# Optimization experiments

Hardware: AMD Instinct MI355X
Metric: run time of the kernel (lower is better)

Reference implementation:

```python
import jax, jax.numpy as jnp
import numpy as np
from jax import lax

DILATIONS = (1, 3, 9, 27, 81, 1)
C = 128        # model channels
UP = 2048      # up-projection channels
K = 512        # filterbank kernel size
NZ = 64        # non_zero_elements kept by sparsify
B = 2
N = 32768      # n_samples


def conv1d(x, w, b, dilation=1, padding='VALID'):
    # x: [B,Cin,T], w: [Cout,Cin,Kw]
    y = lax.conv_general_dilated(x, w, (1,), padding, rhs_dilation=(dilation,),
                                 dimension_numbers=('NCH', 'OIH', 'NCH'))
    return y if b is None else y + b[None, :, None]


def dilated_stack(x, ws, bs, causal_past):
    # residual stack of kernel-2 dilated causal convs; 'only-past' pads left, 'only-future' pads right
    for i, d in enumerate(DILATIONS):
        pad = ((0, 0), (0, 0), (d, 0)) if causal_past else ((0, 0), (0, 0), (0, d))
        h = conv1d(jnp.pad(x, pad), ws[i], bs[i], dilation=d)
        x = x + jax.nn.leaky_relu(h, 0.2)
    return x


def sparsify_topk(x, k):
    # keep top-k values (soft=True: keep magnitudes) over flattened (C,T) per sample
    b = x.shape[0]
    flat = x.reshape(b, -1)
    vals, idx = lax.top_k(flat, k)
    out = jnp.zeros_like(flat).at[jnp.arange(b)[:, None], idx].set(vals)
    return out.reshape(x.shape)


def setup_inputs() -> dict:
    key = jax.random.key(0)
    ks = jax.random.split(key, 11)
    s = 0.1  # weight_init
    return {
        'x': jax.random.normal(ks[0], (B, 1, N), jnp.float32),
        'fb': jax.random.normal(ks[1], (C, 1, K), jnp.float32) * s,        # filterbank
        'enc_w': jax.random.normal(ks[2], (6, C, C, 2), jnp.float32) * s,
        'enc_b': jnp.zeros((6, C), jnp.float32),
        'up_w': jax.random.normal(ks[3], (UP, C, 1), jnp.float32) * s,
        'up_b': jnp.zeros((UP,), jnp.float32),
        'down_w': jax.random.normal(ks[4], (C, UP, 1), jnp.float32) * s,
        'down_b': jnp.zeros((C,), jnp.float32),
        'dec_w': jax.random.normal(ks[5], (6, C, C, 2), jnp.float32) * s,
        'dec_b': jnp.zeros((6, C), jnp.float32),
    }


def reference(x, fb, enc_w, enc_b, up_w, up_b, down_w, down_b, dec_w, dec_b):
    # filterbank analysis: [B,1,N] -> [B,C,N]
    spec = conv1d(x, fb, None, 1, ((K // 2, K // 2 - 1),))
    enc = dilated_stack(spec, enc_w, enc_b, causal_past=False)  # 'only-future'
    enc = conv1d(enc, up_w, up_b)            # [B,2048,N]
    enc = sparsify_topk(enc, NZ)             # 64 nonzeros per sample
    enc = conv1d(enc, down_w, down_b)        # [B,128,N]
    dec = dilated_stack(enc, dec_w, dec_b, causal_past=True)    # 'only-past'
    dec = jnp.pad(dec, ((0, 0), (0, 0), (0, 1)))                # F.pad(decoded, (0,1))
    # transposed convolve back to waveform: flipped filterbank, sum over channels
    kt = jnp.flip(fb, -1).transpose(1, 0, 2)  # [1,C,K]
    final = conv1d(dec, kt, None, 1, ((K // 2 - 1, K // 2),))[:, :, :N]
    return final
```

## Files before the change

kernel.cpp:

```cpp
#include <hip/hip_runtime.h>
#include <stdint.h>

#define NB  2
#define NC  128
#define NT  32768
#define KFB 512
#define NUP 2048
#define CAP 14336

typedef unsigned int u32;
typedef unsigned short u16;
typedef short s16;
typedef float f32x4 __attribute__((ext_vector_type(4)));
typedef s16 short8 __attribute__((ext_vector_type(8)));
typedef u32 u32x4 __attribute__((ext_vector_type(4)));
typedef u32 u32x2 __attribute__((ext_vector_type(2)));

__device__ __forceinline__ u32 f2key(float v){
  u32 u = __float_as_uint(v);
  return (u & 0x80000000u) ? ~u : (u | 0x80000000u);
}
__device__ __forceinline__ float key2f(u32 k){
  u32 u = (k & 0x80000000u) ? (k & 0x7FFFFFFFu) : ~k;
  return __uint_as_float(u);
}
__device__ __forceinline__ u16 bf16rn(float v){
  u32 u = __float_as_uint(v);
  return (u16)((u + 0x7FFFu + ((u>>16)&1u)) >> 16);
}
__device__ __forceinline__ u32 packhl(float v){
  u16 h = bf16rn(v);
  u16 lo = bf16rn(v - __uint_as_float(((u32)h)<<16));
  return ((u32)h<<16) | lo;
}

#define RSH 136

__global__ __launch_bounds__(256) void k_prep(const float* __restrict__ encw,
    const float* __restrict__ decw, const float* __restrict__ upw,
    const float* __restrict__ fbw,
    u16* __restrict__ wdil, u16* __restrict__ wup, u16* __restrict__ wfb,
    u32* __restrict__ h1, u32* __restrict__ h2, int* __restrict__ counts){
  int g = blockIdx.x*256 + threadIdx.x;
  if (g < 2048) h1[g] = 0u;
  else if (g < 4096) h2[g-2048] = 0u;
  if (g < NB) counts[g] = 0;
  if (g < 49152){
    int l = g & 63, mt = (g>>6)&7, s = (g>>9)&7, layer = g>>12;
    const float* W = (layer < 6) ? (encw + (size_t)layer*NC*NC*2)
                                 : (decw + (size_t)(layer-6)*NC*NC*2);
    int co = mt*16 + (l & 15);
    int kb = s*32 + ((l>>4)<<3);
    union { u16 h[8]; u32x4 q; } H, L;
    #pragma unroll
    for (int j=0;j<8;++j){
      int k = kb + j;
      float v = W[((size_t)co*NC + (k&127))*2 + (k>>7)];
      u16 h = bf16rn(v);
      H.h[j] = h;
      L.h[j] = bf16rn(v - __uint_as_float(((u32)h)<<16));
    }
    int unit = g >> 6;
    *(u32x4*)(wdil + (size_t)unit*1024 + (l<<3)) = H.q;
    *(u32x4*)(wdil + (size_t)unit*1024 + 512 + (l<<3)) = L.q;
  } else if (g < 81920){
    int g2 = g - 49152;
    int l = g2 & 63, umt = (g2>>6)&127, s = g2>>13;
    int u = umt*16 + (l & 15);
    int kb = s*32 + ((l>>4)<<3);
    union { u16 h[8]; u32x4 q; } H, L;
    #pragma unroll
    for (int j=0;j<8;++j){
      float v = upw[(size_t)u*NC + kb + j];
      u16 h = bf16rn(v);
      H.h[j] = h;
      L.h[j] = bf16rn(v - __uint_as_float(((u32)h)<<16));
    }
    int unit = g2 >> 6;
    *(u32x4*)(wup + (size_t)unit*1024 + (l<<3)) = H.q;
    *(u32x4*)(wup + (size_t)unit*1024 + 512 + (l<<3)) = L.q;
  } else if (g < 90112){
    int g3 = g - 81920;
    int l = g3 & 63, mt = (g3>>6)&7, s = g3>>9;
    int c = mt*16 + (l & 15);
    int kb = s*32 + ((l>>4)<<3);
    union { u16 h[8]; u32x4 q; } H, L;
    #pragma unroll
    for (int j=0;j<8;++j){
      float v = fbw[(size_t)c*KFB + kb + j];
      u16 h = bf16rn(v);
      H.h[j] = h;
      L.h[j] = bf16rn(v - __uint_as_float(((u32)h)<<16));
    }
    int unit = g3 >> 6;
    *(u32x4*)(wfb + (size_t)unit*1024 + (l<<3)) = H.q;
    *(u32x4*)(wfb + (size_t)unit*1024 + 512 + (l<<3)) = L.q;
  }
}

__global__ __launch_bounds__(256) void k_fb(const float* __restrict__ x,
    const u16* __restrict__ wfb, float* __restrict__ spec){
  __shared__ u32 xw[640];
  const int tid = threadIdx.x;
  const int t0 = blockIdx.x << 7;
  const int b  = blockIdx.y;
  const int lane = tid & 63, w = tid >> 6;
  const int wy = w >> 1, wx = w & 1;
  const int quad = lane >> 4, l15 = lane & 15;
  for (int i = tid; i < 640; i += 256){
    int t = t0 - 256 + i;
    float v = ((u32)t < (u32)NT) ? x[b*NT + t] : 0.0f;
    xw[i] = packhl(v);
  }
  __syncthreads();
  f32x4 acc[4][4] = {};
  for (int s = 0; s < 16; ++s){
    short8 ah[4], al[4];
    #pragma unroll
    for (int mt=0; mt<4; ++mt){
      const u16* p = wfb + (size_t)(s*8 + wy*4 + mt)*1024 + (lane<<3);
      ah[mt] = *(const short8*)p;
      al[mt] = *(const short8*)(p + 512);
    }
    short8 xh[4], xl[4];
    #pragma unroll
    for (int nt=0; nt<4; ++nt){
      int base = s*32 + quad*8 + (wx<<6) + (nt<<4) + l15;
      u32 r[8];
      #pragma unroll
      for (int j=0;j<8;++j) r[j] = xw[base + j];
      union { u32 u[4]; short8 v; } H, L;
      H.u[0] = __builtin_amdgcn_perm(r[1], r[0], 0x07060302u);
      H.u[1] = __builtin_amdgcn_perm(r[3], r[2], 0x07060302u);
      H.u[2] = __builtin_amdgcn_perm(r[5], r[4], 0x07060302u);
      H.u[3] = __builtin_amdgcn_perm(r[7], r[6], 0x07060302u);
      L.u[0] = __builtin_amdgcn_perm(r[1], r[0], 0x05040100u);
      L.u[1] = __builtin_amdgcn_perm(r[3], r[2], 0x05040100u);
      L.u[2] = __builtin_amdgcn_perm(r[5], r[4], 0x05040100u);
      L.u[3] = __builtin_amdgcn_perm(r[7], r[6], 0x05040100u);
      xh[nt] = H.v; xl[nt] = L.v;
    }
    #pragma unroll
    for (int mt=0; mt<4; ++mt){
      #pragma unroll
      for (int nt=0; nt<4; ++nt){
        acc[mt][nt] = __builtin_amdgcn_mfma_f32_16x16x32_bf16(ah[mt], xh[nt], acc[mt][nt], 0,0,0);
        acc[mt][nt] = __builtin_amdgcn_mfma_f32_16x16x32_bf16(ah[mt], xl[nt], acc[mt][nt], 0,0,0);
        acc[mt][nt] = __builtin_amdgcn_mfma_f32_16x16x32_bf16(al[mt], xh[nt], acc[mt][nt], 0,0,0);
      }
    }
  }
  #pragma unroll
  for (int mt=0; mt<4; ++mt){
    #pragma unroll
    for (int r=0; r<4; ++r){
      const int c = (wy<<6) + (mt<<4) + (quad<<2) + r;
      float* po = spec + (size_t)(b*NC+c)*NT + t0 + (wx<<6) + l15;
      #pragma unroll
      for (int nt=0; nt<4; ++nt) po[nt<<4] = acc[mt][nt][r];
    }
  }
}

__global__ __launch_bounds__(1024,4) void k_stack(const float* __restrict__ xin,
    float* __restrict__ xout, const u16* __restrict__ wf,
    const float* __restrict__ biases, int mode){
  extern __shared__ u16 ls[];
  u16* lh = ls;
  u16* ll = ls + 256*RSH;
  const int tid = threadIdx.x;
  const int b  = blockIdx.y;
  const int T0 = blockIdx.x << 7;
  const int row0g = mode ? (T0 - 122) : T0;
  const int lane = tid & 63, w = tid >> 6;
  const int wm = w >> 2, wn = w & 3;
  const int quad = lane >> 4, l15 = lane & 15;
  {
    const float* xb = xin + (size_t)b*NC*NT;
    const int row = tid & 255;
    const int ci0 = (tid >> 8) << 5;
    const int tg = row0g + row;
    const bool ok = ((u32)tg < (u32)NT);
    const float* src = xb + (size_t)ci0*NT + tg;
    u16* dh = lh + row*RSH + ci0;
    u16* dl = ll + row*RSH + ci0;
    #pragma unroll
    for (int g=0; g<4; ++g){
      union { u16 h[8]; short8 v; } H, L;
      #pragma unroll
      for (int j=0;j<8;++j){
        float v = ok ? src[(size_t)(g*8 + j)*NT] : 0.0f;
        u16 hh = bf16rn(v);
        H.h[j] = hh;
        L.h[j] = bf16rn(v - __uint_as_float(((u32)hh)<<16));
      }
      *(short8*)(dh + (g<<3)) = H.v;
      *(short8*)(dl + (g<<3)) = L.v;
    }
  }
  const int dils[6] = {1,3,9,27,81,1};
  const int Hrem[6] = {121,118,109,82,1,0};
  #pragma unroll 1
  for (int l = 0; l < 6; ++l){
    const int d = dils[l];
    const int o0 = mode ? -d : 0;
    const int o1 = mode ? 0 : d;
    const int lo = mode ? (122 - Hrem[l]) : 0;
    const int hi = mode ? 250 : (128 + Hrem[l]);
    const u16* wl = wf + ((size_t)l << 16);
    __syncthreads();
    bool act[4];
    #pragma unroll
    for (int nt=0;nt<4;++nt){
      const int Tst = (wn<<6) + (nt<<4);
      act[nt] = (Tst + 16 > lo) && (Tst < hi);
    }
    f32x4 acc[2][4] = {};
    short8 cah[2], cal[2], nah[2], nal[2];
    {
      const u16* p0 = wl + (size_t)(((wm<<1) + 0) << 10) + (lane<<3);
      const u16* p1 = wl + (size_t)(((wm<<1) + 1) << 10) + (lane<<3);
      cah[0] = *(const short8*)p0; cal[0] = *(const short8*)(p0 + 512);
      cah[1] = *(const short8*)p1; cal[1] = *(const short8*)(p1 + 512);
    }
    #pragma unroll 1
    for (int s = 0; s < 8; ++s){
      const int sn = (s < 7) ? (s + 1) : 7;
      const u16* p0 = wl + (size_t)(((sn<<3) + (wm<<1) + 0) << 10) + (lane<<3);
      const u16* p1 = wl + (size_t)(((sn<<3) + (wm<<1) + 1) << 10) + (lane<<3);
      nah[0] = *(const short8*)p0; nal[0] = *(const short8*)(p0 + 512);
      nah[1] = *(const short8*)p1; nal[1] = *(const short8*)(p1 + 512);
      const int o = (s >= 4) ? o1 : o0;
      const int cig = (s & 3) << 5;
      #pragma unroll
      for (int nt=0;nt<4;++nt){
        if (!act[nt]) continue;
        const int T = ((wn<<6) + (nt<<4) + l15 + o) & 255;
        const int base = T*RSH + cig + (quad<<3);
        short8 xh = *(const short8*)&lh[base];
        short8 xl = *(const short8*)&ll[base];
        acc[0][nt] = __builtin_amdgcn_mfma_f32_16x16x32_bf16(cah[0], xh, acc[0][nt], 0,0,0);
        acc[0][nt] = __builtin_amdgcn_mfma_f32_16x16x32_bf16(cah[0], xl, acc[0][nt], 0,0,0);
        acc[0][nt] = __builtin_amdgcn_mfma_f32_16x16x32_bf16(cal[0], xh, acc[0][nt], 0,0,0);
        acc[1][nt] = __builtin_amdgcn_mfma_f32_16x16x32_bf16(cah[1], xh, acc[1][nt], 0,0,0);
        acc[1][nt] = __builtin_amdgcn_mfma_f32_16x16x32_bf16(cah[1], xl, acc[1][nt], 0,0,0);
        acc[1][nt] = __builtin_amdgcn_mfma_f32_16x16x32_bf16(cal[1], xh, acc[1][nt], 0,0,0);
      }
      cah[0] = nah[0]; cal[0] = nal[0];
      cah[1] = nah[1]; cal[1] = nal[1];
    }
    __syncthreads();
    const float* bl = biases + l*NC;
    const bool last = (l == 5);
    #pragma unroll
    for (int mt=0;mt<2;++mt){
      const int cobase = (wm<<5) + (mt<<4) + (quad<<2);
      float bv[4];
      #pragma unroll
      for (int r=0;r<4;++r) bv[r] = bl[cobase + r];
      #pragma unroll
      for (int nt=0;nt<4;++nt){
        if (!act[nt]) continue;
        const int T = (wn<<6) + (nt<<4) + l15;
        const int base = T*RSH + cobase;
        union { u16 h[4]; u32x2 q; } HH, LL;
        HH.q = *(const u32x2*)&lh[base];
        LL.q = *(const u32x2*)&ll[base];
        const int tg = row0g + T;
        const bool tvld = ((u32)tg < (u32)NT);
        float nv[4];
        #pragma unroll
        for (int r=0;r<4;++r){
          float oldv = __uint_as_float(((u32)HH.h[r])<<16) + __uint_as_float(((u32)LL.h[r])<<16);
          float h = acc[mt][nt][r] + bv[r];
          h = (h >= 0.f) ? h : 0.2f*h;
          float xn = oldv + h;
          nv[r] = tvld ? xn : 0.0f;
        }
        if (!last){
          #pragma unroll
          for (int r=0;r<4;++r){
            u16 hh = bf16rn(nv[r]);
            HH.h[r] = hh;
            LL.h[r] = bf16rn(nv[r] - __uint_as_float(((u32)hh)<<16));
          }
          *(u32x2*)&lh[base] = HH.q;
          *(u32x2*)&ll[base] = LL.q;
        } else {
          const bool rowok = mode ? (T >= 122 && T < 250) : (T < 128);
          if (rowok){
            float* po = xout + (size_t)(b*NC + cobase)*NT + tg;
            #pragma unroll
            for (int r=0;r<4;++r) po[(size_t)r*NT] = nv[r];
          }
        }
      }
    }
  }
}

__global__ __launch_bounds__(256) void k_sub(const float* __restrict__ enc,
                                             const float* __restrict__ upw,
                                             const float* __restrict__ upb,
                                             u32* __restrict__ keys,
                                             u32* __restrict__ hist1){
  const int u0 = blockIdx.x * 64;
  const int i0 = blockIdx.y * 256;
  const int b  = blockIdx.z;
  __shared__ float uwl[32][68];
  __shared__ float ec[32][260];
  __shared__ u32 lh[1024];
  const int tid = threadIdx.x;
  for (int i=tid;i<1024;i+=256) lh[i] = 0u;
  const int ug = tid & 15;
  const int ig = tid >> 4;
  float acc[4][16];
  #pragma unroll
  for (int i=0;i<4;++i){
    #pragma unroll
    for (int j=0;j<16;++j) acc[i][j]=0.0f;
  }
  for (int c0=0;c0<NC;c0+=32){
    __syncthreads();
    #pragma unroll
    for (int i=0;i<8;++i){
      int flat = i*256+tid;
      uwl[flat & 31][flat >> 5] = upw[(size_t)(u0 + (flat>>5))*NC + c0 + (flat&31)];
    }
    #pragma unroll
    for (int i=0;i<32;++i){
      int flat = i*256+tid;
      ec[flat >> 8][flat & 255] = enc[(size_t)(b*NC + c0 + (flat>>8))*NT + (size_t)(i0 + (flat&255))*32];
    }
    __syncthreads();
    #pragma unroll 2
    for (int cc=0;cc<32;++cc){
      float a[4], bb[16];
      *(float4*)&a[0] = *(const float4*)&uwl[cc][ug*4];
      #pragma unroll
      for (int m=0;m<4;++m)
        *(float4*)&bb[m*4] = *(const float4*)&ec[cc][ig*16 + m*4];
      #pragma unroll
      for (int i=0;i<4;++i){
        #pragma unroll
        for (int j=0;j<16;++j)
          acc[i][j] = fmaf(a[i], bb[j], acc[i][j]);
      }
    }
  }
  #pragma unroll
  for (int i=0;i<4;++i){
    int u = u0 + ug*4 + i;
    float ub = upb[u];
    #pragma unroll
    for (int j=0;j<16;++j){
      float v = acc[i][j] + ub;
      u32 k = f2key(v);
      keys[(size_t)(b*NUP + u)*1024 + i0 + ig*16 + j] = k;
      atomicAdd(&lh[k >> 22], 1u);
    }
  }
  __syncthreads();
  for (int i=tid;i<1024;i+=256){
    u32 c = lh[i];
    if (c) atomicAdd(&hist1[b*1024 + i], c);
  }
}

__global__ __launch_bounds__(256) void k_sel(const u32* __restrict__ hist,
                                             u32* __restrict__ cstar,
                                             u32* __restrict__ nab,
                                             u32* __restrict__ t0key,
                                             int phase){
  const int b = blockIdx.x;
  __shared__ u32 s1[1024];
  __shared__ u32 s2[1024];
  __shared__ int red[256];
  const int tid = threadIdx.x;
  for (int i=tid;i<1024;i+=256) s1[i] = hist[b*1024 + i];
  __syncthreads();
  u32* cur = s1; u32* nxt = s2;
  for (int off=1; off<1024; off<<=1){
    for (int i=tid;i<1024;i+=256){
      u32 v = cur[i];
      if (i + off < 1024) v += cur[i+off];
      nxt[i] = v;
    }
    __syncthreads();
    u32* t = cur; cur = nxt; nxt = t;
  }
  u32 off0 = (phase==1) ? 0u : nab[b];
  int best = -1;
  for (int i=tid;i<1024;i+=256)
    if (off0 + cur[i] >= 64u && i > best) best = i;
  red[tid] = best;
  __syncthreads();
  for (int st=128; st>0; st>>=1){
    if (tid < st) red[tid] = max(red[tid], red[tid+st]);
    __syncthreads();
  }
  if (tid == 0){
    int bi = (red[0] < 0) ? 0 : red[0];
    if (phase == 1){
      cstar[b] = (u32)bi;
      nab[b] = (bi < 1023) ? cur[bi+1] : 0u;
    } else {
      t0key[b] = (cstar[b] << 22) | (((u32)bi) << 12);
    }
  }
}

__global__ void k_h2(const u32* __restrict__ keys, const u32* __restrict__ cstar,
                     u32* __restrict__ hist2){
  const u32 c0 = cstar[0], c1 = cstar[1];
  int i = blockIdx.x*256 + threadIdx.x;
  const int total = NB*NUP*1024;
  const int stride = gridDim.x*256;
  for (; i < total; i += stride){
    u32 k = keys[i];
    u32 cs = (i >> 21) ? c1 : c0;
    if ((k >> 22) == cs) atomicAdd(&hist2[((u32)(i>>21)<<10) + ((k>>12) & 1023u)], 1u);
  }
}

__global__ __launch_bounds__(256,2) void k_up(const float* __restrict__ enc,
    const u16* __restrict__ wf, const float* __restrict__ upb,
    const u32* __restrict__ t0key, float* __restrict__ cval,
    int* __restrict__ cidx, int* __restrict__ counts){
  extern __shared__ u16 ls[];
  u16* lh = ls;
  u16* ll = ls + 128*RSH;
  const int tid = threadIdx.x;
  const int t0 = blockIdx.x << 7;
  const int b  = blockIdx.y;
  const int lane = tid & 63, w = tid >> 6;
  const int wy = w >> 1, wx = w & 1;
  const int quad = lane >> 4, l15 = lane & 15;
  {
    const float* xb = enc + (size_t)b*NC*NT + t0;
    const int row = tid >> 1;
    const int ci0 = (tid & 1) << 6;
    const float* src = xb + (size_t)ci0*NT + row;
    u16* dh = lh + row*RSH + ci0;
    u16* dl = ll + row*RSH + ci0;
    #pragma unroll
    for (int g=0; g<8; ++g){
      union { u16 h[8]; short8 v; } H, L;
      #pragma unroll
      for (int j=0;j<8;++j){
        float v = src[(size_t)(g*8 + j)*NT];
        u16 hh = bf16rn(v);
        H.h[j] = hh;
        L.h[j] = bf16rn(v - __uint_as_float(((u32)hh)<<16));
      }
      *(short8*)(dh + (g<<3)) = H.v;
      *(short8*)(dl + (g<<3)) = L.v;
    }
  }
  __syncthreads();
  float T0 = key2f(t0key[b]);
  T0 -= fabsf(T0)*3e-4f + 1e-5f;
  short8 cah[4], cal[4], nah[4], nal[4];
  {
    #pragma unroll
    for (int mt=0;mt<4;++mt){
      const u16* p = wf + (size_t)((wy*4 + mt) << 10) + (lane<<3);
      cah[mt] = *(const short8*)p; cal[mt] = *(const short8*)(p + 512);
    }
  }
  f32x4 acc[4][4] = {};
  #pragma unroll 1
  for (int ss = 0; ss < 64; ++ss){
    const int uc = ss >> 2, s = ss & 3;
    const int ssn = (ss < 63) ? (ss + 1) : 63;
    const int ucn = ssn >> 2, sn = ssn & 3;
    #pragma unroll
    for (int mt=0;mt<4;++mt){
      const u16* p = wf + (size_t)((sn*128 + ucn*8 + wy*4 + mt) << 10) + (lane<<3);
      nah[mt] = *(const short8*)p; nal[mt] = *(const short8*)(p + 512);
    }
    const int cig = s << 5;
    #pragma unroll
    for (int nt=0;nt<4;++nt){
      const int T = (wx<<6) + (nt<<4) + l15;
      const int base = T*RSH + cig + (quad<<3);
      short8 xh = *(const short8*)&lh[base];
      short8 xl = *(const short8*)&ll[base];
      #pragma unroll
      for (int mt=0;mt<4;++mt){
        acc[mt][nt] = __builtin_amdgcn_mfma_f32_16x16x32_bf16(cah[mt], xh, acc[mt][nt], 0,0,0);
        acc[mt][nt] = __builtin_amdgcn_mfma_f32_16x16x32_bf16(cah[mt], xl, acc[mt][nt], 0,0,0);
        acc[mt][nt] = __builtin_amdgcn_mfma_f32_16x16x32_bf16(cal[mt], xh, acc[mt][nt], 0,0,0);
      }
    }
    if (s == 3){
      #pragma unroll
      for (int mt=0; mt<4; ++mt){
        #pragma unroll
        for (int r=0; r<4; ++r){
          int u = uc*128 + (wy<<6) + (mt<<4) + (quad<<2) + r;
          float ub = upb[u];
          #pragma unroll
          for (int nt=0; nt<4; ++nt){
            float v = acc[mt][nt][r] + ub;
            if (v >= T0){
              int slot = atomicAdd(&counts[b], 1);
              if (slot < CAP){
                cval[b*CAP + slot] = v;
                cidx[b*CAP + slot] = u*NT + (t0 + (wx<<6) + (nt<<4) + l15);
              }
            }
          }
        }
      }
      #pragma unroll
      for (int mt=0;mt<4;++mt)
        #pragma unroll
        for (int nt=0;nt<4;++nt) acc[mt][nt] = (f32x4){0.f,0.f,0.f,0.f};
    }
    #pragma unroll
    for (int mt=0;mt<4;++mt){ cah[mt] = nah[mt]; cal[mt] = nal[mt]; }
  }
}

__global__ __launch_bounds__(256) void k_top(const float* __restrict__ cval,
                                             const int* __restrict__ cidx,
                                             const int* __restrict__ counts,
                                             float* __restrict__ tv,
                                             int* __restrict__ ti){
  const int b = blockIdx.x;
  __shared__ float lv[CAP];
  __shared__ float sv[256];
  __shared__ int   si[256];
  const int tid = threadIdx.x;
  int n = counts[b]; if (n > CAP) n = CAP;
  if (n <= 4096){
    float v[16];
    #pragma unroll
    for (int r=0;r<16;++r){
      int i = r*256 + tid;
      v[r] = (i < n) ? cval[b*CAP+i] : -3.4e38f;
    }
    const int lane = tid & 63, wv = tid >> 6;
    for (int r=0;r<64;++r){
      float best = v[0]; int bidx = 0;
      #pragma unroll
      for (int k=1;k<16;++k){ if (v[k] > best){ best = v[k]; bidx = k; } }
      int gi = bidx*256 + tid;
      #pragma unroll
      for (int off=32; off>0; off>>=1){
        float ov = __shfl_down(best, off);
        int oi = __shfl_down(gi, off);
        if (ov > best){ best = ov; gi = oi; }
      }
      if (lane == 0){ sv[wv] = best; si[wv] = gi; }
      __syncthreads();
      if (tid == 0){
        float bb = sv[0]; int bbi = si[0];
        #pragma unroll
        for (int k=1;k<4;++k) if (sv[k] > bb){ bb = sv[k]; bbi = si[k]; }
        si[4] = bbi;
        if (bb > -3.0e38f){ tv[b*64+r] = bb; ti[b*64+r] = cidx[b*CAP + bbi]; }
        else { tv[b*64+r] = 0.0f; ti[b*64+r] = 0; }
      }
      __syncthreads();
      int wini = si[4];
      if ((wini & 255) == tid) v[wini >> 8] = -3.4e38f;
    }
  } else {
    for (int i=tid;i<n;i+=256) lv[i] = cval[b*CAP+i];
    __syncthreads();
    for (int r=0;r<64;++r){
      float best = -3.4e38f; int bi = -1;
      for (int i=tid;i<n;i+=256){
        float v = lv[i];
        if (v > best){ best = v; bi = i; }
      }
      sv[tid]=best; si[tid]=bi;
      __syncthreads();
      for (int st=128; st>0; st>>=1){
        if (tid < st && sv[tid+st] > sv[tid]){ sv[tid]=sv[tid+st]; si[tid]=si[tid+st]; }
        __syncthreads();
      }
      if (tid == 0){
        int kb = si[0];
        if (kb >= 0){
          tv[b*64+r] = sv[0];
          ti[b*64+r] = cidx[b*CAP+kb];
          lv[kb] = -3.4e38f;
        } else { tv[b*64+r] = 0.0f; ti[b*64+r] = 0; }
      }
      __syncthreads();
    }
  }
}

__global__ void k_dec0(float* __restrict__ dst, const float* __restrict__ dnb,
                       const float* __restrict__ dnw,
                       const float* __restrict__ tv, const int* __restrict__ ti){
  const int b = blockIdx.x >> 7, c = blockIdx.x & 127;
  float v = dnb[c];
  float4 vv; vv.x=v; vv.y=v; vv.z=v; vv.w=v;
  float* row = dst + (size_t)(b*NC+c)*NT;
  for (int i=threadIdx.x; i < NT/4; i += 256) *(float4*)&row[i*4] = vv;
  __syncthreads();
  if (threadIdx.x < 64){
    int r = threadIdx.x;
    float sv = tv[b*64+r];
    int idx = ti[b*64+r];
    int u = idx / NT, t = idx - u*NT;
    atomicAdd(&row[t], dnw[(size_t)c*NUP + u] * sv);
  }
}

#define TS 4096
__global__ __launch_bounds__(256) void k_syn(const float* __restrict__ dec,
                                             const float* __restrict__ fb,
                                             float* __restrict__ part){
  const int ts = blockIdx.x;
  const int c  = blockIdx.y;
  const int b  = blockIdx.z;
  const int t0 = ts * TS;
  __shared__ float win2[16*289 + 8];
  __shared__ float fbl[512];
  const int tid = threadIdx.x;
  const int tl = tid * 16;
  float acc[16];
  #pragma unroll
  for (int j=0;j<16;++j) acc[j] = 0.0f;
  for (int i=tid; i < TS+511; i += 256){
    int t = t0 - 255 + i;
    win2[(i & 15)*289 + (i >> 4)] = ((u32)t < (u32)NT) ? dec[(size_t)(b*NC+c)*NT + t] : 0.0f;
  }
  for (int i=tid; i<512; i+=256) fbl[i] = fb[c*KFB + i];
  __syncthreads();
  float w[23];
  #pragma unroll
  for (int k=0;k<23;++k){
    int i = tl + 504 + k;
    w[k] = win2[(i & 15)*289 + (i >> 4)];
  }
  for (int G=0; G<64; ++G){
    float4 f0 = *(const float4*)&fbl[G*8];
    float4 f1 = *(const float4*)&fbl[G*8+4];
    float fq[8] = {f0.x, f0.y, f0.z, f0.w, f1.x, f1.y, f1.z, f1.w};
    #pragma unroll
    for (int q=0;q<8;++q){
      #pragma unroll
      for (int jj=0;jj<16;++jj)
        acc[jj] = fmaf(fq[q], w[7-q+jj], acc[jj]);
    }
    if (G != 63){
      #pragma unroll
      for (int k=22;k>=8;--k) w[k] = w[k-8];
      #pragma unroll
      for (int k=0;k<8;++k){
        int i = tl + 496 - 8*G + k;
        w[k] = win2[(i & 15)*289 + (i >> 4)];
      }
    }
  }
  float* po = &part[(size_t)(c*NB + b)*NT + t0 + tl];
  #pragma unroll
  for (int m=0;m<4;++m){
    float4 ov; ov.x=acc[m*4+0]; ov.y=acc[m*4+1]; ov.z=acc[m*4+2]; ov.w=acc[m*4+3];
    *(float4*)&po[m*4] = ov;
  }
}

__global__ void k_red(const float* __restrict__ part, float* __restrict__ out){
  int i4 = blockIdx.x*256 + threadIdx.x;
  float4 s; s.x=0.f; s.y=0.f; s.z=0.f; s.w=0.f;
  #pragma unroll 4
  for (int c=0;c<128;++c){
    float4 p = *(const float4*)&part[(size_t)c*(NB*NT) + (size_t)i4*4];
    s.x += p.x; s.y += p.y; s.z += p.z; s.w += p.w;
  }
  *(float4*)&out[(size_t)i4*4] = s;
}

extern "C" void kernel_launch(void* const* d_in, const int* in_sizes, int n_in,
                              void* d_out, int out_size, void* d_ws, size_t ws_size,
                              hipStream_t stream){
  const float* x    = (const float*)d_in[0];
  const float* fb   = (const float*)d_in[1];
  const float* encw = (const float*)d_in[2];
  const float* encb = (const float*)d_in[3];
  const float* upw  = (const float*)d_in[4];
  const float* upb  = (const float*)d_in[5];
  const float* dnw  = (const float*)d_in[6];
  const float* dnb  = (const float*)d_in[7];
  const float* decw = (const float*)d_in[8];
  const float* decb = (const float*)d_in[9];
  float* out = (float*)d_out;
  char* ws = (char*)d_ws;

  size_t o = 0;
  float* bufA = (float*)(ws + o); o += (size_t)NB*NC*NT*4;
  float* bufB = (float*)(ws + o); o += (size_t)NB*NC*NT*4;
  u32*  keys  = (u32*)(ws + o);   o += (size_t)NB*NUP*1024*4;
  u32*  hist1 = (u32*)(ws + o);   o += 1024*NB*4;
  u32*  hist2 = (u32*)(ws + o);   o += 1024*NB*4;
  u32*  cstar = (u32*)(ws + o);   o += 64;
  u32*  nab   = (u32*)(ws + o);   o += 64;
  u32*  t0k   = (u32*)(ws + o);   o += 64;
  int*  cnt   = (int*)(ws + o);   o += 64;
  float* tv   = (float*)(ws + o); o += NB*64*4;
  int*  ti    = (int*)(ws + o);   o += NB*64*4;
  float* cval = (float*)(ws + o); o += (size_t)NB*CAP*4;
  int*  cidx  = (int*)(ws + o);   o += (size_t)NB*CAP*4;
  u16*  wdil  = (u16*)(ws + o);   o += (size_t)12*65536*2;
  u16*  wup   = (u16*)(ws + o);   o += (size_t)4*128*1024*2;
  u16*  wfb   = (u16*)(ws + o);   o += (size_t)128*1024*2;
  float* part = bufA;

  k_prep<<<dim3(352), dim3(256), 0, stream>>>(encw, decw, upw, fb, wdil, wup, wfb, hist1, hist2, cnt);
  k_fb<<<dim3(256,NB), dim3(256), 0, stream>>>(x, wfb, bufA);

  k_stack<<<dim3(256,NB), dim3(1024), 2*256*RSH*2, stream>>>(bufA, bufB, wdil, encb, 0);

  k_sub<<<dim3(32,4,NB), dim3(256), 0, stream>>>(bufB, upw, upb, keys, hist1);
  k_sel<<<dim3(NB), dim3(256), 0, stream>>>(hist1, cstar, nab, t0k, 1);
  k_h2 <<<dim3(4096), dim3(256), 0, stream>>>(keys, cstar, hist2);
  k_sel<<<dim3(NB), dim3(256), 0, stream>>>(hist2, cstar, nab, t0k, 2);
  k_up <<<dim3(256,NB), dim3(256), 2*128*RSH*2, stream>>>(bufB, wup, upb, t0k, cval, cidx, cnt);
  k_top<<<dim3(NB), dim3(256), 0, stream>>>(cval, cidx, cnt, tv, ti);

  k_dec0<<<dim3(NB*NC), dim3(256), 0, stream>>>(bufA, dnb, dnw, tv, ti);

  k_stack<<<dim3(256,NB), dim3(1024), 2*256*RSH*2, stream>>>(bufA, bufB, wdil + (size_t)6*65536, decb, 1);

  k_syn<<<dim3(8,128,NB), dim3(256), 0, stream>>>(bufB, fb, part);
  k_red<<<dim3(64), dim3(256), 0, stream>>>(part, out);
}
```

Before: 821.7 us.

## Interleave hi/lo bf16 pairs in stack LDS, enlarge synthesis tiles and top-k buffer

k_stack now keeps each activation as one packed 32-bit hi/lo bf16 word in a single LDS array with row stride 132. Operands are split back into hi and lo vectors with perm instructions, which replaces two separate LDS reads with wider vector loads. k_syn doubles its time tile to 8192 with 512-thread blocks, halving the grid and the halo reloads. k_top's register fast path now handles up to 8192 candidates, at the cost of more VGPRs and extra perm ALU work in the inner loop.

```diff
diff --git a/kernel.cpp b/kernel.cpp
--- a/kernel.cpp
+++ b/kernel.cpp
@@ -14,7 +14,6 @@
 typedef float f32x4 __attribute__((ext_vector_type(4)));
 typedef s16 short8 __attribute__((ext_vector_type(8)));
 typedef u32 u32x4 __attribute__((ext_vector_type(4)));
-typedef u32 u32x2 __attribute__((ext_vector_type(2)));
 
 __device__ __forceinline__ u32 f2key(float v){
   u32 u = __float_as_uint(v);
@@ -33,8 +32,22 @@
   u16 lo = bf16rn(v - __uint_as_float(((u32)h)<<16));
   return ((u32)h<<16) | lo;
 }
-
-#define RSH 136
+__device__ __forceinline__ void unpack8(const u32* p, short8& xh, short8& xl){
+  u32x4 r0 = *(const u32x4*)p;
+  u32x4 r1 = *(const u32x4*)(p + 4);
+  union { u32 u[4]; short8 v; } H, L;
+  H.u[0] = __builtin_amdgcn_perm(r0.y, r0.x, 0x07060302u);
+  H.u[1] = __builtin_amdgcn_perm(r0.w, r0.z, 0x07060302u);
+  H.u[2] = __builtin_amdgcn_perm(r1.y, r1.x, 0x07060302u);
+  H.u[3] = __builtin_amdgcn_perm(r1.w, r1.z, 0x07060302u);
+  L.u[0] = __builtin_amdgcn_perm(r0.y, r0.x, 0x05040100u);
+  L.u[1] = __builtin_amdgcn_perm(r0.w, r0.z, 0x05040100u);
+  L.u[2] = __builtin_amdgcn_perm(r1.y, r1.x, 0x05040100u);
+  L.u[3] = __builtin_amdgcn_perm(r1.w, r1.z, 0x05040100u);
+  xh = H.v; xl = L.v;
+}
+
+#define RS 132
 
 __global__ __launch_bounds__(256) void k_prep(const float* __restrict__ encw,
     const float* __restrict__ decw, const float* __restrict__ upw,
@@ -165,9 +178,7 @@
 __global__ __launch_bounds__(1024,4) void k_stack(const float* __restrict__ xin,
     float* __restrict__ xout, const u16* __restrict__ wf,
     const float* __restrict__ biases, int mode){
-  extern __shared__ u16 ls[];
-  u16* lh = ls;
-  u16* ll = ls + 256*RSH;
+  extern __shared__ u32 lx[];
   const int tid = threadIdx.x;
   const int b  = blockIdx.y;
   const int T0 = blockIdx.x << 7;
@@ -182,20 +193,16 @@
     const int tg = row0g + row;
     const bool ok = ((u32)tg < (u32)NT);
     const float* src = xb + (size_t)ci0*NT + tg;
-    u16* dh = lh + row*RSH + ci0;
-    u16* dl = ll + row*RSH + ci0;
-    #pragma unroll
-    for (int g=0; g<4; ++g){
-      union { u16 h[8]; short8 v; } H, L;
-      #pragma unroll
-      for (int j=0;j<8;++j){
-        float v = ok ? src[(size_t)(g*8 + j)*NT] : 0.0f;
-        u16 hh = bf16rn(v);
-        H.h[j] = hh;
-        L.h[j] = bf16rn(v - __uint_as_float(((u32)hh)<<16));
-      }
-      *(short8*)(dh + (g<<3)) = H.v;
-      *(short8*)(dl + (g<<3)) = L.v;
+    u32* dst = lx + row*RS + ci0;
+    #pragma unroll
+    for (int g=0; g<8; ++g){
+      u32x4 q;
+      #pragma unroll
+      for (int k=0;k<4;++k){
+        float v = ok ? src[(size_t)(g*4 + k)*NT] : 0.0f;
+        q[k] = packhl(v);
+      }
+      *(u32x4*)(dst + g*4) = q;
     }
   }
   const int dils[6] = {1,3,9,27,81,1};
@@ -236,9 +243,9 @@
       for (int nt=0;nt<4;++nt){
         if (!act[nt]) continue;
         const int T = ((wn<<6) + (nt<<4) + l15 + o) & 255;
-        const int base = T*RSH + cig + (quad<<3);
-        short8 xh = *(const short8*)&lh[base];
-        short8 xl = *(const short8*)&ll[base];
+        const int idx = T*RS + cig + (quad<<3);
+        short8 xh, xl;
+        unpack8(&lx[idx], xh, xl);
         acc[0][nt] = __builtin_amdgcn_mfma_f32_16x16x32_bf16(cah[0], xh, acc[0][nt], 0,0,0);
         acc[0][nt] = __builtin_amdgcn_mfma_f32_16x16x32_bf16(cah[0], xl, acc[0][nt], 0,0,0);
         acc[0][nt] = __builtin_amdgcn_mfma_f32_16x16x32_bf16(cal[0], xh, acc[0][nt], 0,0,0);
@@ -262,30 +269,24 @@
       for (int nt=0;nt<4;++nt){
         if (!act[nt]) continue;
         const int T = (wn<<6) + (nt<<4) + l15;
-        const int base = T*RSH + cobase;
-        union { u16 h[4]; u32x2 q; } HH, LL;
-        HH.q = *(const u32x2*)&lh[base];
-        LL.q = *(const u32x2*)&ll[base];
+        const int idx = T*RS + cobase;
+        u32x4 xo = *(const u32x4*)&lx[idx];
         const int tg = row0g + T;
         const bool tvld = ((u32)tg < (u32)NT);
         float nv[4];
         #pragma unroll
         for (int r=0;r<4;++r){
-          float oldv = __uint_as_float(((u32)HH.h[r])<<16) + __uint_as_float(((u32)LL.h[r])<<16);
+          float oldv = __uint_as_float(xo[r] & 0xFFFF0000u) + __uint_as_float(xo[r] << 16);
           float h = acc[mt][nt][r] + bv[r];
           h = (h >= 0.f) ? h : 0.2f*h;
           float xn = oldv + h;
           nv[r] = tvld ? xn : 0.0f;
         }
         if (!last){
+          u32x4 np;
           #pragma unroll
-          for (int r=0;r<4;++r){
-            u16 hh = bf16rn(nv[r]);
-            HH.h[r] = hh;
-            LL.h[r] = bf16rn(nv[r] - __uint_as_float(((u32)hh)<<16));
-          }
-          *(u32x2*)&lh[base] = HH.q;
-          *(u32x2*)&ll[base] = LL.q;
+          for (int r=0;r<4;++r) np[r] = packhl(nv[r]);
+          *(u32x4*)&lx[idx] = np;
         } else {
           const bool rowok = mode ? (T >= 122 && T < 250) : (T < 128);
           if (rowok){
@@ -423,13 +424,14 @@
   }
 }
 
+#define RSH 136
 __global__ __launch_bounds__(256,2) void k_up(const float* __restrict__ enc,
     const u16* __restrict__ wf, const float* __restrict__ upb,
     const u32* __restrict__ t0key, float* __restrict__ cval,
     int* __restrict__ cidx, int* __restrict__ counts){
   extern __shared__ u16 ls[];
-  u16* lh = ls;
-  u16* ll = ls + 128*RSH;
+  u16* lhh = ls;
+  u16* lll = ls + 128*RSH;
   const int tid = threadIdx.x;
   const int t0 = blockIdx.x << 7;
   const int b  = blockIdx.y;
@@ -441,8 +443,8 @@
     const int row = tid >> 1;
     const int ci0 = (tid & 1) << 6;
     const float* src = xb + (size_t)ci0*NT + row;
-    u16* dh = lh + row*RSH + ci0;
-    u16* dl = ll + row*RSH + ci0;
+    u16* dh = lhh + row*RSH + ci0;
+    u16* dl = lll + row*RSH + ci0;
     #pragma unroll
     for (int g=0; g<8; ++g){
       union { u16 h[8]; short8 v; } H, L;
@@ -484,8 +486,8 @@
     for (int nt=0;nt<4;++nt){
       const int T = (wx<<6) + (nt<<4) + l15;
       const int base = T*RSH + cig + (quad<<3);
-      short8 xh = *(const short8*)&lh[base];
-      short8 xl = *(const short8*)&ll[base];
+      short8 xh = *(const short8*)&lhh[base];
+      short8 xl = *(const short8*)&lll[base];
       #pragma unroll
       for (int mt=0;mt<4;++mt){
         acc[mt][nt] = __builtin_amdgcn_mfma_f32_16x16x32_bf16(cah[mt], xh, acc[mt][nt], 0,0,0);
@@ -534,10 +536,10 @@
   __shared__ int   si[256];
   const int tid = threadIdx.x;
   int n = counts[b]; if (n > CAP) n = CAP;
-  if (n <= 4096){
-    float v[16];
-    #pragma unroll
-    for (int r=0;r<16;++r){
+  if (n <= 8192){
+    float v[32];
+    #pragma unroll
+    for (int r=0;r<32;++r){
       int i = r*256 + tid;
       v[r] = (i < n) ? cval[b*CAP+i] : -3.4e38f;
     }
@@ -545,7 +547,7 @@
     for (int r=0;r<64;++r){
       float best = v[0]; int bidx = 0;
       #pragma unroll
-      for (int k=1;k<16;++k){ if (v[k] > best){ best = v[k]; bidx = k; } }
+      for (int k=1;k<32;++k){ if (v[k] > best){ best = v[k]; bidx = k; } }
       int gi = bidx*256 + tid;
       #pragma unroll
       for (int off=32; off>0; off>>=1){
@@ -613,32 +615,33 @@
   }
 }
 
-#define TS 4096
-__global__ __launch_bounds__(256) void k_syn(const float* __restrict__ dec,
+#define TS 8192
+#define WR 545
+__global__ __launch_bounds__(512) void k_syn(const float* __restrict__ dec,
                                              const float* __restrict__ fb,
                                              float* __restrict__ part){
   const int ts = blockIdx.x;
   const int c  = blockIdx.y;
   const int b  = blockIdx.z;
   const int t0 = ts * TS;
-  __shared__ float win2[16*289 + 8];
+  __shared__ float win2[16*WR];
   __shared__ float fbl[512];
   const int tid = threadIdx.x;
   const int tl = tid * 16;
   float acc[16];
   #pragma unroll
   for (int j=0;j<16;++j) acc[j] = 0.0f;
-  for (int i=tid; i < TS+511; i += 256){
+  for (int i=tid; i < TS+511; i += 512){
     int t = t0 - 255 + i;
-    win2[(i & 15)*289 + (i >> 4)] = ((u32)t < (u32)NT) ? dec[(size_t)(b*NC+c)*NT + t] : 0.0f;
-  }
-  for (int i=tid; i<512; i+=256) fbl[i] = fb[c*KFB + i];
+    win2[(i & 15)*WR + (i >> 4)] = ((u32)t < (u32)NT) ? dec[(size_t)(b*NC+c)*NT + t] : 0.0f;
+  }
+  if (tid < 512) fbl[tid] = fb[c*KFB + tid];
   __syncthreads();
   float w[23];
   #pragma unroll
   for (int k=0;k<23;++k){
     int i = tl + 504 + k;
-    w[k] = win2[(i & 15)*289 + (i >> 4)];
+    w[k] = win2[(i & 15)*WR + (i >> 4)];
   }
   for (int G=0; G<64; ++G){
     float4 f0 = *(const float4*)&fbl[G*8];
@@ -656,7 +659,7 @@
       #pragma unroll
       for (int k=0;k<8;++k){
         int i = tl + 496 - 8*G + k;
-        w[k] = win2[(i & 15)*289 + (i >> 4)];
+        w[k] = win2[(i & 15)*WR + (i >> 4)];
       }
     }
   }
@@ -717,7 +720,7 @@
   k_prep<<<dim3(352), dim3(256), 0, stream>>>(encw, decw, upw, fb, wdil, wup, wfb, hist1, hist2, cnt);
   k_fb<<<dim3(256,NB), dim3(256), 0, stream>>>(x, wfb, bufA);
 
-  k_stack<<<dim3(256,NB), dim3(1024), 2*256*RSH*2, stream>>>(bufA, bufB, wdil, encb, 0);
+  k_stack<<<dim3(256,NB), dim3(1024), 256*RS*4, stream>>>(bufA, bufB, wdil, encb, 0);
 
   k_sub<<<dim3(32,4,NB), dim3(256), 0, stream>>>(bufB, upw, upb, keys, hist1);
   k_sel<<<dim3(NB), dim3(256), 0, stream>>>(hist1, cstar, nab, t0k, 1);
@@ -728,8 +731,8 @@
 
   k_dec0<<<dim3(NB*NC), dim3(256), 0, stream>>>(bufA, dnb, dnw, tv, ti);
 
-  k_stack<<<dim3(256,NB), dim3(1024), 2*256*RSH*2, stream>>>(bufA, bufB, wdil + (size_t)6*65536, decb, 1);
-
-  k_syn<<<dim3(8,128,NB), dim3(256), 0, stream>>>(bufB, fb, part);
+  k_stack<<<dim3(256,NB), dim3(1024), 256*RS*4, stream>>>(bufA, bufB, wdil + (size_t)6*65536, decb, 1);
+
+  k_syn<<<dim3(4,128,NB), dim3(512), 0, stream>>>(bufB, fb, part);
   k_red<<<dim3(64), dim3(256), 0, stream>>>(part, out);
 }
```

New measurement: 906.4 us. 1.1x slower.
